# Kernel tuning notes

Measured on AMD Instinct MI355X. Metric: run time of the kernel, lower is better.

The kernel has to match this reference:

```python
import jax, jax.numpy as jnp
import numpy as np

N, E, H, C, F_IN = 10000, 160000, 8, 128, 4  # nodes, edges, heads, per-head dim, input feats
D = H * C  # 1024 concat dim


def _gelu(v):
    return jax.nn.gelu(v, approximate=False)  # torch F.gelu default is exact erf


def _gat(x, src, dst, w, a_s, a_d, b):
    """PyG GATConv (concat=True, negative_slope=0.2), self-loops already in src/dst."""
    n = x.shape[0]
    h = (x @ w).reshape(n, H, C)                      # [N,H,C]
    e = (h * a_s).sum(-1)[src] + (h * a_d).sum(-1)[dst]  # [E,H] per-edge logits
    e = jnp.where(e > 0, e, 0.2 * e)                  # LeakyReLU(0.2)
    m = jax.lax.stop_gradient(jax.ops.segment_max(e, dst, num_segments=n))
    p = jnp.exp(e - m[dst])
    z = jax.ops.segment_sum(p, dst, num_segments=n)   # [N,H]
    alpha = p / z[dst]                                # softmax over incoming edges
    out = jax.ops.segment_sum(h[src] * alpha[:, :, None], dst, num_segments=n)
    return out.reshape(n, D) + b


def setup_inputs() -> dict:
    key = jax.random.key(0)
    ks = jax.random.split(key, 24)
    s = 0.05
    inp = {
        "x": jax.random.normal(ks[0], (N, F_IN), dtype=jnp.float32),
        "edge_index": jax.random.randint(ks[1], (2, E), 0, N),
        "w1": jax.random.normal(ks[2], (F_IN, D)) * s,
        "asrc1": jax.random.normal(ks[3], (H, C)) * s,
        "adst1": jax.random.normal(ks[4], (H, C)) * s,
        "bias1": jnp.zeros((D,), jnp.float32),
        "w2": jax.random.normal(ks[5], (C, D)) * s,
        "asrc2": jax.random.normal(ks[6], (H, C)) * s,
        "adst2": jax.random.normal(ks[7], (H, C)) * s,
        "bias2": jnp.zeros((D,), jnp.float32),
        "w3": jax.random.normal(ks[8], (C, D)) * s,
        "asrc3": jax.random.normal(ks[9], (H, C)) * s,
        "adst3": jax.random.normal(ks[10], (H, C)) * s,
        "bias3": jnp.zeros((D,), jnp.float32),
        "rw1": jax.random.normal(ks[11], (D, C)) * s,
        "rb1": jnp.zeros((C,), jnp.float32),
        "rw2": jax.random.normal(ks[12], (D, C)) * s,
        "rb2": jnp.zeros((C,), jnp.float32),
        "lw": jax.random.normal(ks[13], (D, C)) * s,
        "lb": jnp.zeros((C,), jnp.float32),
    }
    return inp


def reference(x, edge_index, w1, asrc1, adst1, bias1, w2, asrc2, adst2, bias2,
              w3, asrc3, adst3, bias3, rw1, rb1, rw2, rb2, lw, lb):
    loops = jnp.arange(N, dtype=edge_index.dtype)
    src = jnp.concatenate([edge_index[0], loops])
    dst = jnp.concatenate([edge_index[1], loops])
    h = _gat(x, src, dst, w1, asrc1, adst1, bias1)            # [N, 1024]
    h = _gat(_gelu(h) @ rw1 + rb1, src, dst, w2, asrc2, adst2, bias2)
    h = _gat(_gelu(h) @ rw2 + rb2, src, dst, w3, asrc3, adst3, bias3)
    return _gelu(h) @ lw + lb                                 # [N, 128]
```

## Files before the change

kernel.cpp:

```cpp
#include <hip/hip_runtime.h>
#include <hip/hip_fp16.h>
#include <math.h>


#define THREADS 256
#define CAP 128

typedef _Float16 f16x8 __attribute__((ext_vector_type(8)));
typedef float f32x4 __attribute__((ext_vector_type(4)));

struct __align__(8) Half4 { __half2 a, b; };

__device__ __forceinline__ float gelu_exact(float x) {
  return 0.5f * x * (1.0f + erff(x * 0.70710678118654752f));
}


__global__ __launch_bounds__(256) void prep_kernel(
    const int* __restrict__ ei, int E, int ET, int* __restrict__ counts,
    const float* __restrict__ w2, const float* __restrict__ w3,
    const float* __restrict__ rw1, const float* __restrict__ rw2,
    const float* __restrict__ lw,
    __half* __restrict__ wt2, __half* __restrict__ wt3,
    __half* __restrict__ rwt1, __half* __restrict__ rwt2,
    __half* __restrict__ lwt,
    const float* __restrict__ w1,
    const float* __restrict__ as1, const float* __restrict__ ad1,
    const float* __restrict__ as2, const float* __restrict__ ad2,
    const float* __restrict__ as3, const float* __restrict__ ad3,
    float* __restrict__ ws1, float* __restrict__ wd1,
    float* __restrict__ ws2, float* __restrict__ wd2,
    float* __restrict__ ws3, float* __restrict__ wd3,
    int nHist) {
  __shared__ float tile[32][33];
  int bid = blockIdx.x;
  int t = threadIdx.x;

  if (bid < nHist) {
    int e = bid * 256 + t;
    if (e >= ET) return;
    int d = (e < E) ? ei[E + e] : (e - E);
    atomicAdd(&counts[d], 1);
    return;
  }
  bid -= nHist;
  if (bid < 640) {
    const float* in; __half* out; int K, Ncol;
    int z = bid >> 7, rem = bid & 127;
    switch (z) {
      case 0: in = w2;  out = wt2;  K = 128;  Ncol = 1024; break;
      case 1: in = w3;  out = wt3;  K = 128;  Ncol = 1024; break;
      case 2: in = rw1; out = rwt1; K = 1024; Ncol = 128;  break;
      case 3: in = rw2; out = rwt2; K = 1024; Ncol = 128;  break;
      default: in = lw; out = lwt;  K = 1024; Ncol = 128;  break;
    }
    int kt, ct;
    if (z < 2) { kt = rem >> 5; ct = rem & 31; }
    else       { kt = rem & 31; ct = rem >> 5; }
    int kb = kt * 32, cb = ct * 32;
    int tc = t & 31, tr = t >> 5;
#pragma unroll
    for (int r = tr; r < 32; r += 8)
      tile[r][tc] = in[(size_t)(kb + r) * Ncol + cb + tc];
    __syncthreads();
#pragma unroll
    for (int r = tr; r < 32; r += 8)
      out[(size_t)(cb + r) * K + kb + tc] = __float2half_rn(tile[tc][r]);
    return;
  }
  bid -= 640;
  {
    int h = bid & 7, yy = bid >> 3;
    int sel = t >> 7;
    int k = t & 127;
    const float* W; const float* av; float* outp; int K;
    switch (yy) {
      case 0: W = w2; av = sel ? ad2 : as2; outp = sel ? wd2 : ws2; K = 128; break;
      case 1: W = w3; av = sel ? ad3 : as3; outp = sel ? wd3 : ws3; K = 128; break;
      default: W = w1; av = sel ? ad1 : as1; outp = sel ? wd1 : ws1; K = 4; break;
    }
    if (k >= K) return;
    const float* wrow = W + (size_t)k * 1024 + h * 128;
    const float* arow = av + h * 128;
    float s = 0.f;
    for (int c = 0; c < 128; c += 4) {
      float4 wv = *(const float4*)&wrow[c];
      float4 a4 = *(const float4*)&arow[c];
      s += wv.x * a4.x + wv.y * a4.y + wv.z * a4.z + wv.w * a4.w;
    }
    outp[h * K + k] = s;
  }
}


__global__ __launch_bounds__(1024) void scan_scores_kernel(
    const int* __restrict__ counts, int* __restrict__ offsets,
    int* __restrict__ cursor, int n,
    const float* __restrict__ x,
    const float* __restrict__ ws1, const float* __restrict__ wd1,
    float* __restrict__ ssrc, float* __restrict__ sdst, int total) {
  __shared__ int sums[1024];
  if (blockIdx.x == 0) {
    int t = threadIdx.x;
    int per = (n + 1023) >> 10;
    int start = t * per; if (start > n) start = n;
    int end = start + per; if (end > n) end = n;
    int local = 0;
    for (int i = start; i < end; ++i) local += counts[i];
    sums[t] = local;
    __syncthreads();
    for (int off = 1; off < 1024; off <<= 1) {
      int add = (t >= off) ? sums[t - off] : 0;
      __syncthreads();
      sums[t] += add;
      __syncthreads();
    }
    int run = (t == 0) ? 0 : sums[t - 1];
    for (int i = start; i < end; ++i) {
      offsets[i] = run; cursor[i] = run; run += counts[i];
    }
    if (t == 1023) offsets[n] = run;
    return;
  }
  int idx = (blockIdx.x - 1) * 1024 + threadIdx.x;
  if (idx >= total) return;
  int nn = idx >> 3, h = idx & 7;
  float4 xv = *(const float4*)&x[nn * 4];
  float4 a = *(const float4*)&ws1[h * 4];
  float4 b = *(const float4*)&wd1[h * 4];
  ssrc[idx] = xv.x * a.x + xv.y * a.y + xv.z * a.z + xv.w * a.w;
  sdst[idx] = xv.x * b.x + xv.y * b.y + xv.z * b.z + xv.w * b.w;
}

__global__ void scatter_kernel(const int* __restrict__ ei, int E, int ET,
                               int* __restrict__ cursor, int* __restrict__ srcs) {
  int e = blockIdx.x * THREADS + threadIdx.x;
  if (e >= ET) return;
  int s = (e < E) ? ei[e] : (e - E);
  int d = (e < E) ? ei[E + e] : (e - E);
  int pos = atomicAdd(&cursor[d], 1);
  srcs[pos] = s;
}


__global__ __launch_bounds__(256) void attnagg_p(const __half* __restrict__ P16,
                                                 const int* __restrict__ srcs,
                                                 const int* __restrict__ offsets,
                                                 const float* __restrict__ ssrc,
                                                 const float* __restrict__ sdst,
                                                 __half* __restrict__ Y16, int NP) {
  __shared__ float lal[4][CAP][8];
  __shared__ int ls[4][CAP];
  __shared__ float szinv[4][8];
  int w = threadIdx.x >> 6, lane = threadIdx.x & 63;
  int n = blockIdx.x * 4 + w;
  int start = offsets[n], deg = offsets[n + 1] - start;
  int head = lane & 7, es = lane >> 3;
  float sd = sdst[n * 8 + head];
  int c2 = lane * 2;
  const __half* pbase = P16 + c2;
  float accx[8] = {}, accy[8] = {};
  float s = 0.f;
  for (int cc = 0; cc < deg; cc += CAP) {
    int cm = min(CAP, deg - cc);
    for (int i = es; i < cm; i += 8) {
      int sp = srcs[start + cc + i];
      float v = ssrc[sp * 8 + head] + sd;
      v = (v > 0.f) ? v : 0.2f * v;
      float e = __expf(v);
      lal[w][i][head] = e;
      if (head == 0) ls[w][i] = sp;
      s += e;
    }
    int i = 0;
    for (; i + 8 <= cm; i += 8) {
      float2 pv[8];
#pragma unroll
      for (int u = 0; u < 8; ++u) {
        int sp = ls[w][i + u];
        pv[u] = __half22float2(*(const __half2*)&pbase[(size_t)sp * 128]);
      }
#pragma unroll
      for (int u = 0; u < 8; ++u) {
        float4 a00 = *(float4*)&lal[w][i + u][0];
        float4 a01 = *(float4*)&lal[w][i + u][4];
        float a0[8] = {a00.x, a00.y, a00.z, a00.w, a01.x, a01.y, a01.z, a01.w};
#pragma unroll
        for (int h = 0; h < 8; ++h) {
          accx[h] += a0[h] * pv[u].x; accy[h] += a0[h] * pv[u].y;
        }
      }
    }
    for (; i < cm; ++i) {
      int sp0 = ls[w][i];
      float2 p0 = __half22float2(*(const __half2*)&pbase[(size_t)sp0 * 128]);
      float4 a00 = *(float4*)&lal[w][i][0];
      float4 a01 = *(float4*)&lal[w][i][4];
      float a0[8] = {a00.x, a00.y, a00.z, a00.w, a01.x, a01.y, a01.z, a01.w};
#pragma unroll
      for (int h = 0; h < 8; ++h) {
        accx[h] += a0[h] * p0.x; accy[h] += a0[h] * p0.y;
      }
    }
  }
#pragma unroll
  for (int mask = 8; mask <= 32; mask <<= 1)
    s += __shfl_xor(s, mask);
  if (es == 0) szinv[w][head] = 1.f / s;
#pragma unroll
  for (int h = 0; h < 8; ++h) {
    float zi = szinv[w][h];
    *(__half2*)&Y16[((size_t)h * NP + n) * 128 + c2] =
        __floats2half2_rn(accx[h] * zi, accy[h] * zi);
  }
}


__global__ __launch_bounds__(256) void attnagg_x(const float* __restrict__ x,
                                                 const int* __restrict__ srcs,
                                                 const int* __restrict__ offsets,
                                                 const float* __restrict__ ssrc,
                                                 const float* __restrict__ sdst,
                                                 float* __restrict__ Y1, int NP) {
  __shared__ float lal[4][CAP][8];
  __shared__ int ls[4][CAP];
  __shared__ float szinv[4][8];
  int w = threadIdx.x >> 6, lane = threadIdx.x & 63;
  int n = blockIdx.x * 4 + w;
  int start = offsets[n], deg = offsets[n + 1] - start;
  int head = lane & 7, es = lane >> 3;
  float sd = sdst[n * 8 + head];
  int eo = lane >> 5, hb = (lane >> 2) & 7, ch = lane & 3;
  float acc = 0.f;
  float s = 0.f;
  for (int cc = 0; cc < deg; cc += CAP) {
    int cm = min(CAP, deg - cc);
    for (int i = es; i < cm; i += 8) {
      int sp = srcs[start + cc + i];
      float v = ssrc[sp * 8 + head] + sd;
      v = (v > 0.f) ? v : 0.2f * v;
      float e = __expf(v);
      lal[w][i][head] = e;
      if (head == 0) ls[w][i] = sp;
      s += e;
    }
    int i = eo;
    for (; i + 6 < cm; i += 8) {
      float xv[4]; float av[4];
#pragma unroll
      for (int u = 0; u < 4; ++u) {
        int sp = ls[w][i + 2 * u];
        xv[u] = x[sp * 4 + ch];
      }
#pragma unroll
      for (int u = 0; u < 4; ++u) av[u] = lal[w][i + 2 * u][hb];
#pragma unroll
      for (int u = 0; u < 4; ++u) acc += av[u] * xv[u];
    }
    for (; i < cm; i += 2) {
      int sp = ls[w][i];
      acc += lal[w][i][hb] * x[sp * 4 + ch];
    }
  }
#pragma unroll
  for (int mask = 8; mask <= 32; mask <<= 1)
    s += __shfl_xor(s, mask);
  if (es == 0) szinv[w][head] = 1.f / s;
  acc += __shfl_xor(acc, 32);
  if (lane < 32) {
    float zi = szinv[w][hb];
    Y1[((size_t)hb * NP + n) * 4 + ch] = acc * zi;
  }
}


template <typename OutT, bool SC>
__global__ __launch_bounds__(512) void tail_mfma(const __half* __restrict__ Y16,
                                                 const __half* __restrict__ WtA,
                                                 const float* __restrict__ biasA,
                                                 const __half* __restrict__ WtP,
                                                 const float* __restrict__ biasP,
                                                 OutT* __restrict__ out, int N, int NP,
                                                 const float* __restrict__ wsn,
                                                 const float* __restrict__ wdn,
                                                 float* __restrict__ ssrc,
                                                 float* __restrict__ sdst) {
  __shared__ __half Gt[32][1032];
  __shared__ __half Pl[32][136];
  int w = threadIdx.x >> 6, lane = threadIdx.x & 63;
  int r0 = blockIdx.x * 32;
  int m = lane & 15, quad = lane >> 4;
  {
    int h = w;
    const __half* py0 = Y16 + ((size_t)h * NP + r0 + m) * 128 + quad * 8;
    const __half* py1 = py0 + (size_t)16 * 128;
    f16x8 bf0[4], bf1[4];
#pragma unroll
    for (int kk = 0; kk < 4; ++kk) {
      bf0[kk] = *(const f16x8*)(py0 + kk * 32);
      bf1[kk] = *(const f16x8*)(py1 + kk * 32);
    }
#pragma unroll
    for (int tile = 0; tile < 8; ++tile) {
      int gc = h * 128 + tile * 16;
      const __half* pa = WtA + (size_t)(gc + m) * 128 + quad * 8;
      f16x8 a[4];
#pragma unroll
      for (int kk = 0; kk < 4; ++kk) a[kk] = *(const f16x8*)(pa + kk * 32);
      f32x4 acc0 = {0.f, 0.f, 0.f, 0.f}, acc1 = {0.f, 0.f, 0.f, 0.f};
#pragma unroll
      for (int kk = 0; kk < 4; ++kk) {
        acc0 = __builtin_amdgcn_mfma_f32_16x16x32_f16(a[kk], bf0[kk], acc0, 0, 0, 0);
        acc1 = __builtin_amdgcn_mfma_f32_16x16x32_f16(a[kk], bf1[kk], acc1, 0, 0, 0);
      }
      float4 b4 = *(const float4*)&biasA[gc + quad * 4];
      Half4 p0, p1;
      p0.a = __floats2half2_rn(gelu_exact(acc0[0] + b4.x), gelu_exact(acc0[1] + b4.y));
      p0.b = __floats2half2_rn(gelu_exact(acc0[2] + b4.z), gelu_exact(acc0[3] + b4.w));
      p1.a = __floats2half2_rn(gelu_exact(acc1[0] + b4.x), gelu_exact(acc1[1] + b4.y));
      p1.b = __floats2half2_rn(gelu_exact(acc1[2] + b4.z), gelu_exact(acc1[3] + b4.w));
      *(Half4*)&Gt[m][gc + quad * 4] = p0;
      *(Half4*)&Gt[16 + m][gc + quad * 4] = p1;
    }
  }
  __syncthreads();
  {
    int c0 = w * 16;
    const __half* pa = WtP + (size_t)(c0 + m) * 1024 + quad * 8;
    f32x4 acc0 = {0.f, 0.f, 0.f, 0.f}, acc1 = {0.f, 0.f, 0.f, 0.f};
#pragma unroll 8
    for (int k = 0; k < 1024; k += 32) {
      f16x8 a = *(const f16x8*)(pa + k);
      f16x8 b0 = *(const f16x8*)&Gt[m][quad * 8 + k];
      f16x8 b1 = *(const f16x8*)&Gt[16 + m][quad * 8 + k];
      acc0 = __builtin_amdgcn_mfma_f32_16x16x32_f16(a, b0, acc0, 0, 0, 0);
      acc1 = __builtin_amdgcn_mfma_f32_16x16x32_f16(a, b1, acc1, 0, 0, 0);
    }
    float4 b4 = *(const float4*)&biasP[c0 + quad * 4];
    int row0 = r0 + m, row1 = r0 + 16 + m;
    if constexpr (__is_same(OutT, __half)) {
      Half4 p, q;
      p.a = __floats2half2_rn(acc0[0] + b4.x, acc0[1] + b4.y);
      p.b = __floats2half2_rn(acc0[2] + b4.z, acc0[3] + b4.w);
      q.a = __floats2half2_rn(acc1[0] + b4.x, acc1[1] + b4.y);
      q.b = __floats2half2_rn(acc1[2] + b4.z, acc1[3] + b4.w);
      if constexpr (SC) {
        *(Half4*)&Pl[m][c0 + quad * 4] = p;
        *(Half4*)&Pl[16 + m][c0 + quad * 4] = q;
      }
      if (row0 < N) *(Half4*)&out[(size_t)row0 * 128 + c0 + quad * 4] = p;
      if (row1 < N) *(Half4*)&out[(size_t)row1 * 128 + c0 + quad * 4] = q;
    } else {
      if (row0 < N)
        *(float4*)&out[(size_t)row0 * 128 + c0 + quad * 4] =
            make_float4(acc0[0] + b4.x, acc0[1] + b4.y, acc0[2] + b4.z, acc0[3] + b4.w);
      if (row1 < N)
        *(float4*)&out[(size_t)row1 * 128 + c0 + quad * 4] =
            make_float4(acc1[0] + b4.x, acc1[1] + b4.y, acc1[2] + b4.z, acc1[3] + b4.w);
    }
  }
  if constexpr (SC) {
    __syncthreads();
    int head = lane & 7, es = lane >> 3;
    const float* wsp = wsn + head * 128 + es * 16;
    const float* wdp = wdn + head * 128 + es * 16;
    float wsr[16], wdr[16];
#pragma unroll
    for (int j = 0; j < 16; ++j) { wsr[j] = wsp[j]; wdr[j] = wdp[j]; }
#pragma unroll
    for (int r = 0; r < 4; ++r) {
      int row = w * 4 + r;
      f16x8 p0 = *(const f16x8*)&Pl[row][es * 16];
      f16x8 p1 = *(const f16x8*)&Pl[row][es * 16 + 8];
      float s1 = 0.f, s2 = 0.f;
#pragma unroll
      for (int j = 0; j < 8; ++j) {
        float v = (float)p0[j];
        s1 += v * wsr[j]; s2 += v * wdr[j];
      }
#pragma unroll
      for (int j = 0; j < 8; ++j) {
        float v = (float)p1[j];
        s1 += v * wsr[8 + j]; s2 += v * wdr[8 + j];
      }
#pragma unroll
      for (int mask = 8; mask <= 32; mask <<= 1) {
        s1 += __shfl_xor(s1, mask);
        s2 += __shfl_xor(s2, mask);
      }
      int nn = r0 + row;
      if (es == 0 && nn < N) { ssrc[nn * 8 + head] = s1; sdst[nn * 8 + head] = s2; }
    }
  }
}


template <typename OutT, bool SC>
__global__ __launch_bounds__(512) void tail1_kernel(const float* __restrict__ Y1,
                                                    const float* __restrict__ w,
                                                    const float* __restrict__ biasA,
                                                    const __half* __restrict__ WtP,
                                                    const float* __restrict__ biasP,
                                                    OutT* __restrict__ out, int N, int NP,
                                                    const float* __restrict__ wsn,
                                                    const float* __restrict__ wdn,
                                                    float* __restrict__ ssrc,
                                                    float* __restrict__ sdst) {
  __shared__ __half Gt[32][1032];
  __shared__ __half Pl[32][136];
  int t = threadIdx.x;
  int r0 = blockIdx.x * 32;
  {
    int c0 = (t & 255) * 4;
    int h = c0 >> 7;
    float4 wa = *(const float4*)&w[c0];
    float4 wb = *(const float4*)&w[1024 + c0];
    float4 wc = *(const float4*)&w[2048 + c0];
    float4 wd = *(const float4*)&w[3072 + c0];
    float4 b4 = *(const float4*)&biasA[c0];
#pragma unroll 4
    for (int r = t >> 8; r < 32; r += 2) {
      float4 yv = *(const float4*)&Y1[((size_t)h * NP + r0 + r) * 4];
      float o0 = gelu_exact(yv.x * wa.x + yv.y * wb.x + yv.z * wc.x + yv.w * wd.x + b4.x);
      float o1 = gelu_exact(yv.x * wa.y + yv.y * wb.y + yv.z * wc.y + yv.w * wd.y + b4.y);
      float o2 = gelu_exact(yv.x * wa.z + yv.y * wb.z + yv.z * wc.z + yv.w * wd.z + b4.z);
      float o3 = gelu_exact(yv.x * wa.w + yv.y * wb.w + yv.z * wc.w + yv.w * wd.w + b4.w);
      Half4 p;
      p.a = __floats2half2_rn(o0, o1);
      p.b = __floats2half2_rn(o2, o3);
      *(Half4*)&Gt[r][c0] = p;
    }
  }
  __syncthreads();
  int wv = t >> 6, lane = t & 63;
  int m = lane & 15, quad = lane >> 4;
  {
    int c0 = wv * 16;
    const __half* pa = WtP + (size_t)(c0 + m) * 1024 + quad * 8;
    f32x4 acc0 = {0.f, 0.f, 0.f, 0.f}, acc1 = {0.f, 0.f, 0.f, 0.f};
#pragma unroll 8
    for (int k = 0; k < 1024; k += 32) {
      f16x8 a = *(const f16x8*)(pa + k);
      f16x8 b0 = *(const f16x8*)&Gt[m][quad * 8 + k];
      f16x8 b1 = *(const f16x8*)&Gt[16 + m][quad * 8 + k];
      acc0 = __builtin_amdgcn_mfma_f32_16x16x32_f16(a, b0, acc0, 0, 0, 0);
      acc1 = __builtin_amdgcn_mfma_f32_16x16x32_f16(a, b1, acc1, 0, 0, 0);
    }
    float4 b4 = *(const float4*)&biasP[c0 + quad * 4];
    int row0 = r0 + m, row1 = r0 + 16 + m;
    if constexpr (__is_same(OutT, __half)) {
      Half4 p, q;
      p.a = __floats2half2_rn(acc0[0] + b4.x, acc0[1] + b4.y);
      p.b = __floats2half2_rn(acc0[2] + b4.z, acc0[3] + b4.w);
      q.a = __floats2half2_rn(acc1[0] + b4.x, acc1[1] + b4.y);
      q.b = __floats2half2_rn(acc1[2] + b4.z, acc1[3] + b4.w);
      if constexpr (SC) {
        *(Half4*)&Pl[m][c0 + quad * 4] = p;
        *(Half4*)&Pl[16 + m][c0 + quad * 4] = q;
      }
      if (row0 < N) *(Half4*)&out[(size_t)row0 * 128 + c0 + quad * 4] = p;
      if (row1 < N) *(Half4*)&out[(size_t)row1 * 128 + c0 + quad * 4] = q;
    } else {
      if (row0 < N)
        *(float4*)&out[(size_t)row0 * 128 + c0 + quad * 4] =
            make_float4(acc0[0] + b4.x, acc0[1] + b4.y, acc0[2] + b4.z, acc0[3] + b4.w);
      if (row1 < N)
        *(float4*)&out[(size_t)row1 * 128 + c0 + quad * 4] =
            make_float4(acc1[0] + b4.x, acc1[1] + b4.y, acc1[2] + b4.z, acc1[3] + b4.w);
    }
  }
  if constexpr (SC) {
    __syncthreads();
    int head = lane & 7, es = lane >> 3;
    const float* wsp = wsn + head * 128 + es * 16;
    const float* wdp = wdn + head * 128 + es * 16;
    float wsr[16], wdr[16];
#pragma unroll
    for (int j = 0; j < 16; ++j) { wsr[j] = wsp[j]; wdr[j] = wdp[j]; }
#pragma unroll
    for (int r = 0; r < 4; ++r) {
      int row = wv * 4 + r;
      f16x8 p0 = *(const f16x8*)&Pl[row][es * 16];
      f16x8 p1 = *(const f16x8*)&Pl[row][es * 16 + 8];
      float s1 = 0.f, s2 = 0.f;
#pragma unroll
      for (int j = 0; j < 8; ++j) {
        float v = (float)p0[j];
        s1 += v * wsr[j]; s2 += v * wdr[j];
      }
#pragma unroll
      for (int j = 0; j < 8; ++j) {
        float v = (float)p1[j];
        s1 += v * wsr[8 + j]; s2 += v * wdr[8 + j];
      }
#pragma unroll
      for (int mask = 8; mask <= 32; mask <<= 1) {
        s1 += __shfl_xor(s1, mask);
        s2 += __shfl_xor(s2, mask);
      }
      int nn = r0 + row;
      if (es == 0 && nn < N) { ssrc[nn * 8 + head] = s1; sdst[nn * 8 + head] = s2; }
    }
  }
}


extern "C" void kernel_launch(void* const* d_in, const int* in_sizes, int n_in,
                              void* d_out, int out_size, void* d_ws, size_t ws_size,
                              hipStream_t stream) {
  const float* x   = (const float*)d_in[0];
  const int*   ei  = (const int*)d_in[1];
  const float* w1  = (const float*)d_in[2];
  const float* as1 = (const float*)d_in[3];
  const float* ad1 = (const float*)d_in[4];
  const float* b1  = (const float*)d_in[5];
  const float* w2  = (const float*)d_in[6];
  const float* as2 = (const float*)d_in[7];
  const float* ad2 = (const float*)d_in[8];
  const float* b2  = (const float*)d_in[9];
  const float* w3  = (const float*)d_in[10];
  const float* as3 = (const float*)d_in[11];
  const float* ad3 = (const float*)d_in[12];
  const float* b3  = (const float*)d_in[13];
  const float* rw1 = (const float*)d_in[14];
  const float* rb1 = (const float*)d_in[15];
  const float* rw2 = (const float*)d_in[16];
  const float* rb2 = (const float*)d_in[17];
  const float* lw  = (const float*)d_in[18];
  const float* lb  = (const float*)d_in[19];

  int N = in_sizes[0] / 4;
  int E = in_sizes[1] / 2;
  int ET = E + N;
  int nRow32 = (N + 31) / 32;
  int NP = nRow32 * 32;
  (void)ws_size;

  char* wsb = (char*)d_ws;
  size_t off = 0;
  auto alloc = [&](size_t bytes) -> void* {
    void* p = wsb + off;
    off += (bytes + 255) & ~(size_t)255;
    return p;
  };
  __half* P16  = (__half*)alloc((size_t)N * 128 * 2);
  __half* Y16  = (__half*)alloc((size_t)8 * NP * 128 * 2);
  float*  Y1   = (float*)alloc((size_t)8 * NP * 4 * 4);
  __half* wt2  = (__half*)alloc((size_t)1024 * 128 * 2);
  __half* wt3  = (__half*)alloc((size_t)1024 * 128 * 2);
  __half* rwt1 = (__half*)alloc((size_t)128 * 1024 * 2);
  __half* rwt2 = (__half*)alloc((size_t)128 * 1024 * 2);
  __half* lwt  = (__half*)alloc((size_t)128 * 1024 * 2);
  float* ws1 = (float*)alloc(8 * 4 * 4);
  float* wd1 = (float*)alloc(8 * 4 * 4);
  float* ws2 = (float*)alloc(8 * 128 * 4);
  float* wd2 = (float*)alloc(8 * 128 * 4);
  float* ws3 = (float*)alloc(8 * 128 * 4);
  float* wd3 = (float*)alloc(8 * 128 * 4);
  float* ssrc   = (float*)alloc((size_t)N * 8 * 4);
  float* sdst   = (float*)alloc((size_t)N * 8 * 4);
  int* counts  = (int*)alloc((size_t)N * 4);
  int* offsets = (int*)alloc((size_t)(N + 1) * 4);
  int* cursor  = (int*)alloc((size_t)N * 4);
  int* srcs    = (int*)alloc((size_t)ET * 4);

  dim3 blk(THREADS);
  dim3 blk512(512);
  int nHist = (ET + THREADS - 1) / THREADS;

  hipMemsetAsync(counts, 0, (size_t)N * 4, stream);

  prep_kernel<<<dim3(nHist + 640 + 24), blk, 0, stream>>>(
      ei, E, ET, counts,
      w2, w3, rw1, rw2, lw, wt2, wt3, rwt1, rwt2, lwt,
      w1, as1, ad1, as2, ad2, as3, ad3,
      ws1, wd1, ws2, wd2, ws3, wd3, nHist);

  int total1 = N * 8;
  int nSc = (total1 + 1023) / 1024;
  scan_scores_kernel<<<dim3(1 + nSc), dim3(1024), 0, stream>>>(
      counts, offsets, cursor, N, x, ws1, wd1, ssrc, sdst, total1);

  scatter_kernel<<<dim3(nHist), blk, 0, stream>>>(ei, E, ET, cursor, srcs);

  dim3 gNode4(N / 4);
  dim3 gRow32(nRow32);

  attnagg_x<<<gNode4, blk, 0, stream>>>(x, srcs, offsets, ssrc, sdst, Y1, NP);
  tail1_kernel<__half, true><<<gRow32, blk512, 0, stream>>>(
      Y1, w1, b1, rwt1, rb1, P16, N, NP, ws2, wd2, ssrc, sdst);

  attnagg_p<<<gNode4, blk, 0, stream>>>(P16, srcs, offsets, ssrc, sdst, Y16, NP);
  tail_mfma<__half, true><<<gRow32, blk512, 0, stream>>>(
      Y16, wt2, b2, rwt2, rb2, P16, N, NP, ws3, wd3, ssrc, sdst);

  attnagg_p<<<gNode4, blk, 0, stream>>>(P16, srcs, offsets, ssrc, sdst, Y16, NP);
  tail_mfma<float, false><<<gRow32, blk512, 0, stream>>>(
      Y16, wt3, b3, lwt, lb, (float*)d_out, N, NP, nullptr, nullptr, nullptr, nullptr);
}
```

Baseline: 284.5 us.

## Pre-swizzle fp16 weights into MFMA fragment order and vectorize aggregation accumulators

The weight transpose kernel now writes fp16 weights in a tiled layout that matches the MFMA 16x16x32 operand fragments. Each lane's A-operand load therefore becomes one contiguous, coalesced 16-byte read instead of a strided row access. The attention aggregation kernel also switches its paired float accumulators to 2-wide vectors so the compiler can emit packed FMA instructions. The layout change must stay consistent between the producer and every consumer of these weight buffers.

```diff
diff --git a/kernel.cpp b/kernel.cpp
--- a/kernel.cpp
+++ b/kernel.cpp
@@ -8,6 +8,7 @@
 
 typedef _Float16 f16x8 __attribute__((ext_vector_type(8)));
 typedef float f32x4 __attribute__((ext_vector_type(4)));
+typedef float f32x2 __attribute__((ext_vector_type(2)));
 
 struct __align__(8) Half4 { __half2 a, b; };
 
@@ -54,18 +55,24 @@
       case 3: in = rw2; out = rwt2; K = 1024; Ncol = 128;  break;
       default: in = lw; out = lwt;  K = 1024; Ncol = 128;  break;
     }
-    int kt, ct;
-    if (z < 2) { kt = rem >> 5; ct = rem & 31; }
-    else       { kt = rem & 31; ct = rem >> 5; }
-    int kb = kt * 32, cb = ct * 32;
+    int kt2, ct2;
+    if (z < 2) { kt2 = rem >> 5; ct2 = rem & 31; }
+    else       { kt2 = rem & 31; ct2 = rem >> 5; }
+    int kb = kt2 * 32, cb = ct2 * 32;
+    int KT = K >> 5;
     int tc = t & 31, tr = t >> 5;
 #pragma unroll
     for (int r = tr; r < 32; r += 8)
       tile[r][tc] = in[(size_t)(kb + r) * Ncol + cb + tc];
     __syncthreads();
 #pragma unroll
-    for (int r = tr; r < 32; r += 8)
-      out[(size_t)(cb + r) * K + kb + tc] = __float2half_rn(tile[tc][r]);
+    for (int r = tr; r < 32; r += 8) {
+      int c = cb + r, k = kb + tc;
+      int m = c & 15, ct = c >> 4;
+      int j = k & 7, quad = (k >> 3) & 3, kt = k >> 5;
+      out[((size_t)(ct * KT + kt) * 64 + quad * 16 + m) * 8 + j] =
+          __float2half_rn(tile[tc][r]);
+    }
     return;
   }
   bid -= 640;
@@ -159,7 +166,7 @@
   float sd = sdst[n * 8 + head];
   int c2 = lane * 2;
   const __half* pbase = P16 + c2;
-  float accx[8] = {}, accy[8] = {};
+  f32x2 acc2[8] = {};
   float s = 0.f;
   for (int cc = 0; cc < deg; cc += CAP) {
     int cm = min(CAP, deg - cc);
@@ -174,11 +181,12 @@
     }
     int i = 0;
     for (; i + 8 <= cm; i += 8) {
-      float2 pv[8];
+      f32x2 pp[8];
 #pragma unroll
       for (int u = 0; u < 8; ++u) {
         int sp = ls[w][i + u];
-        pv[u] = __half22float2(*(const __half2*)&pbase[(size_t)sp * 128]);
+        float2 f = __half22float2(*(const __half2*)&pbase[(size_t)sp * 128]);
+        pp[u].x = f.x; pp[u].y = f.y;
       }
 #pragma unroll
       for (int u = 0; u < 8; ++u) {
@@ -186,21 +194,18 @@
         float4 a01 = *(float4*)&lal[w][i + u][4];
         float a0[8] = {a00.x, a00.y, a00.z, a00.w, a01.x, a01.y, a01.z, a01.w};
 #pragma unroll
-        for (int h = 0; h < 8; ++h) {
-          accx[h] += a0[h] * pv[u].x; accy[h] += a0[h] * pv[u].y;
-        }
+        for (int h = 0; h < 8; ++h) acc2[h] += a0[h] * pp[u];
       }
     }
     for (; i < cm; ++i) {
       int sp0 = ls[w][i];
-      float2 p0 = __half22float2(*(const __half2*)&pbase[(size_t)sp0 * 128]);
+      float2 f = __half22float2(*(const __half2*)&pbase[(size_t)sp0 * 128]);
+      f32x2 p0; p0.x = f.x; p0.y = f.y;
       float4 a00 = *(float4*)&lal[w][i][0];
       float4 a01 = *(float4*)&lal[w][i][4];
       float a0[8] = {a00.x, a00.y, a00.z, a00.w, a01.x, a01.y, a01.z, a01.w};
 #pragma unroll
-      for (int h = 0; h < 8; ++h) {
-        accx[h] += a0[h] * p0.x; accy[h] += a0[h] * p0.y;
-      }
+      for (int h = 0; h < 8; ++h) acc2[h] += a0[h] * p0;
     }
   }
 #pragma unroll
@@ -211,7 +216,7 @@
   for (int h = 0; h < 8; ++h) {
     float zi = szinv[w][h];
     *(__half2*)&Y16[((size_t)h * NP + n) * 128 + c2] =
-        __floats2half2_rn(accx[h] * zi, accy[h] * zi);
+        __floats2half2_rn(acc2[h].x * zi, acc2[h].y * zi);
   }
 }
 
@@ -303,10 +308,10 @@
 #pragma unroll
     for (int tile = 0; tile < 8; ++tile) {
       int gc = h * 128 + tile * 16;
-      const __half* pa = WtA + (size_t)(gc + m) * 128 + quad * 8;
+      const __half* pa = WtA + (size_t)(h * 8 + tile) * 2048 + lane * 8;
       f16x8 a[4];
 #pragma unroll
-      for (int kk = 0; kk < 4; ++kk) a[kk] = *(const f16x8*)(pa + kk * 32);
+      for (int kk = 0; kk < 4; ++kk) a[kk] = *(const f16x8*)(pa + kk * 512);
       f32x4 acc0 = {0.f, 0.f, 0.f, 0.f}, acc1 = {0.f, 0.f, 0.f, 0.f};
 #pragma unroll
       for (int kk = 0; kk < 4; ++kk) {
@@ -326,11 +331,11 @@
   __syncthreads();
   {
     int c0 = w * 16;
-    const __half* pa = WtP + (size_t)(c0 + m) * 1024 + quad * 8;
+    const __half* pa = WtP + (size_t)w * 16384 + lane * 8;
     f32x4 acc0 = {0.f, 0.f, 0.f, 0.f}, acc1 = {0.f, 0.f, 0.f, 0.f};
 #pragma unroll 8
     for (int k = 0; k < 1024; k += 32) {
-      f16x8 a = *(const f16x8*)(pa + k);
+      f16x8 a = *(const f16x8*)(pa + k * 16);
       f16x8 b0 = *(const f16x8*)&Gt[m][quad * 8 + k];
       f16x8 b1 = *(const f16x8*)&Gt[16 + m][quad * 8 + k];
       acc0 = __builtin_amdgcn_mfma_f32_16x16x32_f16(a, b0, acc0, 0, 0, 0);
@@ -436,11 +441,11 @@
   int m = lane & 15, quad = lane >> 4;
   {
     int c0 = wv * 16;
-    const __half* pa = WtP + (size_t)(c0 + m) * 1024 + quad * 8;
+    const __half* pa = WtP + (size_t)wv * 16384 + lane * 8;
     f32x4 acc0 = {0.f, 0.f, 0.f, 0.f}, acc1 = {0.f, 0.f, 0.f, 0.f};
 #pragma unroll 8
     for (int k = 0; k < 1024; k += 32) {
-      f16x8 a = *(const f16x8*)(pa + k);
+      f16x8 a = *(const f16x8*)(pa + k * 16);
       f16x8 b0 = *(const f16x8*)&Gt[m][quad * 8 + k];
       f16x8 b1 = *(const f16x8*)&Gt[16 + m][quad * 8 + k];
       acc0 = __builtin_amdgcn_mfma_f32_16x16x32_f16(a, b0, acc0, 0, 0, 0);
```

Measured after the change: 248.9 us. -12.5%, faster.
